# Kernel optimization log

Measured on AMD Instinct MI355X. Metric: run time of the kernel, lower is better.

## Reference

```python
import jax, jax.numpy as jnp
import numpy as np

EPS = 1e-06
K = 4          # hc_mult
D = 2048       # hidden_size
SINKHORN_ITERS = 20


def setup_inputs() -> dict:
    key = jax.random.key(0)
    k1, k2, k3 = jax.random.split(key, 3)
    B, S = 2, 4096
    x = jax.random.normal(k1, (B, S, K, D), dtype=jnp.float32)
    out = jax.random.normal(k2, (B, S, D), dtype=jnp.float32)
    out_dim = (2 + K) * K  # 24
    # matches nn.init.normal_(std=1/sqrt(K*D))
    W = jax.random.normal(k3, (out_dim, K * D), dtype=jnp.float32) / np.sqrt(K * D)
    scale = jnp.ones((3,), dtype=jnp.float32)
    base = jnp.zeros((out_dim,), dtype=jnp.float32)
    return {"x": x, "out": out, "W": W, "scale": scale, "base": base}


def _sinkhorn(m, n_iters=SINKHORN_ITERS, eps=EPS):
    # one priming column normalization, then (n_iters-1) row/col cycles
    m = m / (jnp.sum(m, axis=-2, keepdims=True) + eps)
    for _ in range(max(n_iters - 1, 0)):
        m = m / (jnp.sum(m, axis=-1, keepdims=True) + eps)
        m = m / (jnp.sum(m, axis=-2, keepdims=True) + eps)
    return m


def reference(x, out, W, scale, base):
    out_dtype = x.dtype
    # --- _packed_logits: flatten K streams, RMS-normalize, project (fp32) ---
    flat = x.reshape(*x.shape[:-2], K * D).astype(jnp.float32)      # [B,S,K*D]
    rsqrt = jax.lax.rsqrt(jnp.mean(flat * flat, axis=-1, keepdims=True) + EPS)
    logits = jnp.einsum('bsf,of->bso', flat * rsqrt, W)             # [B,S,24]
    # --- compute_weights: split into pre/post/comb ---
    pre_logit = logits[..., :K] * scale[0] + base[:K]
    post_logit = logits[..., K:2 * K] * scale[1] + base[K:2 * K]
    comb_logit = (logits[..., 2 * K:].reshape(*logits.shape[:-1], K, K) * scale[2]
                  + base[2 * K:].reshape(K, K))
    pre = jax.nn.sigmoid(pre_logit) + EPS                           # [B,S,K]
    post = 2.0 * jax.nn.sigmoid(post_logit)                         # [B,S,K]
    comb = jax.nn.softmax(comb_logit, axis=-1) + EPS                # [B,S,K,K]
    comb = _sinkhorn(comb)                                          # doubly-stochastic
    pre = pre.astype(out_dtype)
    post = post.astype(out_dtype)
    comb = comb.astype(out_dtype)
    # --- collapse: K streams -> 1 via pre weights ---
    collapsed = jnp.sum(pre[..., None] * x, axis=-2)                # [B,S,D]
    # --- expand: write sub-block output back to K streams ---
    write = post[..., None] * out[..., None, :]                     # [B,S,K,D]
    mix = jnp.einsum('bshk,bskd->bshd', comb, x)                    # [B,S,K,D]
    y = write + mix
    return (y, collapsed)
```

## Files before the change

### kernel.cpp

```cpp
#include <hip/hip_runtime.h>


#define EPS 1e-6f
constexpr int K_ = 4, D_ = 2048, KD = 8192, NOUT = 24;
constexpr int NTOK = 2 * 4096;
constexpr int TPB = 512;
constexpr int TOKS = 4;

typedef _Float16 h2 __attribute__((ext_vector_type(2)));

static __device__ __forceinline__ unsigned int pk2(float a, float b) {
    h2 h; h.x = (_Float16)a; h.y = (_Float16)b;
    return __builtin_bit_cast(unsigned int, h);
}

static __device__ __forceinline__ float dot2(unsigned int w, unsigned int x, float c) {
#if __has_builtin(__builtin_amdgcn_fdot2)
    return __builtin_amdgcn_fdot2(__builtin_bit_cast(h2, w),
                                  __builtin_bit_cast(h2, x), c, false);
#else
    h2 hw = __builtin_bit_cast(h2, w), hx = __builtin_bit_cast(h2, x);
    return c + (float)hw.x * (float)hx.x + (float)hw.y * (float)hx.y;
#endif
}

__global__ void conv_w_kernel(const float* __restrict__ W, unsigned int* __restrict__ Wh) {
    int g = blockIdx.x * blockDim.x + threadIdx.x;
    const float* src = W + (size_t)g * 8;
    float4 a = *reinterpret_cast<const float4*>(src);
    float4 b = *reinterpret_cast<const float4*>(src + 4);
    uint4 u;
    u.x = pk2(a.x, a.y); u.y = pk2(a.z, a.w);
    u.z = pk2(b.x, b.y); u.w = pk2(b.z, b.w);
    *reinterpret_cast<uint4*>(Wh + (size_t)g * 4) = u;
}

template <bool FH>
__global__ __launch_bounds__(TPB) void hypermix_kernel(
    const float* __restrict__ x, const float* __restrict__ outp,
    const unsigned int* __restrict__ Wh, const float* __restrict__ Wf,
    const float* __restrict__ scale, const float* __restrict__ base,
    float* __restrict__ y, float* __restrict__ coll)
{
    const int t = threadIdx.x;
    const int w = t >> 6, lane = t & 63;
    const int tk4 = t >> 7, t7 = t & 127;
    const size_t gt0 = (size_t)blockIdx.x * TOKS;

    __shared__ unsigned int xh[TOKS][KD / 2];
    __shared__ float ssred[8];
    __shared__ float lg[TOKS][24];
    __shared__ float wts[TOKS][24];

    {
        const float* xb = x + (gt0 + tk4) * KD + t7 * 4;
        float ss = 0.f;
#pragma unroll 2
        for (int i = 0; i < 16; ++i) {
            float4 v = *reinterpret_cast<const float4*>(xb + i * 512);
            ss += v.x * v.x + v.y * v.y + v.z * v.z + v.w * v.w;
            uint2 p; p.x = pk2(v.x, v.y); p.y = pk2(v.z, v.w);
            *reinterpret_cast<uint2*>(&xh[tk4][i * 256 + t7 * 2]) = p;
        }
#pragma unroll
        for (int m = 1; m < 64; m <<= 1) ss += __shfl_xor(ss, m, 64);
        if (lane == 0) ssred[w] = ss;
    }
    __syncthreads();

    {
        const int r0 = w * 3;
        float acc[3][4];
#pragma unroll
        for (int j = 0; j < 3; ++j)
#pragma unroll
            for (int tt = 0; tt < 4; ++tt) acc[j][tt] = 0.f;

#pragma unroll 2
        for (int it = 0; it < 16; ++it) {
            const int gi = it * 64 + lane;
            uint4 xv0 = *reinterpret_cast<const uint4*>(&xh[0][gi * 4]);
            uint4 xv1 = *reinterpret_cast<const uint4*>(&xh[1][gi * 4]);
            uint4 xv2 = *reinterpret_cast<const uint4*>(&xh[2][gi * 4]);
            uint4 xv3 = *reinterpret_cast<const uint4*>(&xh[3][gi * 4]);
#pragma unroll
            for (int j = 0; j < 3; ++j) {
                if (FH) {
                    uint4 wv = *reinterpret_cast<const uint4*>(
                        Wh + ((size_t)(r0 + j) * 4096 + gi * 4));
                    acc[j][0] = dot2(wv.x, xv0.x, acc[j][0]);
                    acc[j][0] = dot2(wv.y, xv0.y, acc[j][0]);
                    acc[j][0] = dot2(wv.z, xv0.z, acc[j][0]);
                    acc[j][0] = dot2(wv.w, xv0.w, acc[j][0]);
                    acc[j][1] = dot2(wv.x, xv1.x, acc[j][1]);
                    acc[j][1] = dot2(wv.y, xv1.y, acc[j][1]);
                    acc[j][1] = dot2(wv.z, xv1.z, acc[j][1]);
                    acc[j][1] = dot2(wv.w, xv1.w, acc[j][1]);
                    acc[j][2] = dot2(wv.x, xv2.x, acc[j][2]);
                    acc[j][2] = dot2(wv.y, xv2.y, acc[j][2]);
                    acc[j][2] = dot2(wv.z, xv2.z, acc[j][2]);
                    acc[j][2] = dot2(wv.w, xv2.w, acc[j][2]);
                    acc[j][3] = dot2(wv.x, xv3.x, acc[j][3]);
                    acc[j][3] = dot2(wv.y, xv3.y, acc[j][3]);
                    acc[j][3] = dot2(wv.z, xv3.z, acc[j][3]);
                    acc[j][3] = dot2(wv.w, xv3.w, acc[j][3]);
                } else {
                    const float* wr = Wf + (size_t)(r0 + j) * KD + gi * 8;
                    float4 w0 = *reinterpret_cast<const float4*>(wr);
                    float4 w1 = *reinterpret_cast<const float4*>(wr + 4);
                    unsigned int wa = pk2(w0.x, w0.y), wb = pk2(w0.z, w0.w);
                    unsigned int wc = pk2(w1.x, w1.y), wd = pk2(w1.z, w1.w);
                    acc[j][0] = dot2(wa, xv0.x, acc[j][0]);
                    acc[j][0] = dot2(wb, xv0.y, acc[j][0]);
                    acc[j][0] = dot2(wc, xv0.z, acc[j][0]);
                    acc[j][0] = dot2(wd, xv0.w, acc[j][0]);
                    acc[j][1] = dot2(wa, xv1.x, acc[j][1]);
                    acc[j][1] = dot2(wb, xv1.y, acc[j][1]);
                    acc[j][1] = dot2(wc, xv1.z, acc[j][1]);
                    acc[j][1] = dot2(wd, xv1.w, acc[j][1]);
                    acc[j][2] = dot2(wa, xv2.x, acc[j][2]);
                    acc[j][2] = dot2(wb, xv2.y, acc[j][2]);
                    acc[j][2] = dot2(wc, xv2.z, acc[j][2]);
                    acc[j][2] = dot2(wd, xv2.w, acc[j][2]);
                    acc[j][3] = dot2(wa, xv3.x, acc[j][3]);
                    acc[j][3] = dot2(wb, xv3.y, acc[j][3]);
                    acc[j][3] = dot2(wc, xv3.z, acc[j][3]);
                    acc[j][3] = dot2(wd, xv3.w, acc[j][3]);
                }
            }
        }
#pragma unroll
        for (int j = 0; j < 3; ++j)
#pragma unroll
            for (int tt = 0; tt < 4; ++tt) {
                float v = acc[j][tt];
#pragma unroll
                for (int m = 1; m < 64; m <<= 1) v += __shfl_xor(v, m, 64);
                if (lane == 0) lg[tt][r0 + j] = v;
            }
    }
    __syncthreads();

    if (t < 64) {
        const int wtk = t >> 4, idx = t & 15;
        float ss = ssred[2 * wtk] + ssred[2 * wtk + 1];
        float rms = rsqrtf(ss * (1.f / 8192.f) + EPS);
        float s0 = scale[0], s1 = scale[1], s2 = scale[2];
        float cl = lg[wtk][8 + idx] * rms * s2 + base[8 + idx];
        float mx = fmaxf(cl, __shfl_xor(cl, 1, 64));
        mx = fmaxf(mx, __shfl_xor(mx, 2, 64));
        float e = expf(cl - mx);
        float se = e + __shfl_xor(e, 1, 64); se += __shfl_xor(se, 2, 64);
        float m = e / se + EPS;
        float cs = m + __shfl_xor(m, 4, 64); cs += __shfl_xor(cs, 8, 64);
        m = m / (cs + EPS);
#pragma unroll 1
        for (int it = 0; it < 19; ++it) {
            float rs = m + __shfl_xor(m, 1, 64); rs += __shfl_xor(rs, 2, 64);
            m = m / (rs + EPS);
            cs = m + __shfl_xor(m, 4, 64); cs += __shfl_xor(cs, 8, 64);
            m = m / (cs + EPS);
        }
        wts[wtk][8 + idx] = m;
        if (idx < 4) {
            float z = lg[wtk][idx] * rms * s0 + base[idx];
            wts[wtk][idx] = 1.f / (1.f + expf(-z)) + EPS;
        } else if (idx < 8) {
            float z = lg[wtk][idx] * rms * s1 + base[idx];
            wts[wtk][idx] = 2.f / (1.f + expf(-z));
        }
    }
    __syncthreads();

    float pre[4], post[4], cmb[4][4];
#pragma unroll
    for (int k = 0; k < 4; ++k) { pre[k] = wts[tk4][k]; post[k] = wts[tk4][4 + k]; }
#pragma unroll
    for (int h = 0; h < 4; ++h)
#pragma unroll
        for (int k = 0; k < 4; ++k) cmb[h][k] = wts[tk4][8 + h * 4 + k];

    const float* ob = outp + (gt0 + tk4) * D_;
    float* yb = y + (gt0 + tk4) * KD;
    float* cb = coll + (gt0 + tk4) * D_;

#pragma unroll 1
    for (int dj = 0; dj < 4; ++dj) {
        const int d = dj * 512 + t7 * 4;
        float xk[4][4];
#pragma unroll
        for (int k = 0; k < 4; ++k) {
            uint2 p = *reinterpret_cast<const uint2*>(&xh[tk4][k * 1024 + (d >> 1)]);
            h2 h0 = __builtin_bit_cast(h2, p.x), h1 = __builtin_bit_cast(h2, p.y);
            xk[k][0] = (float)h0.x; xk[k][1] = (float)h0.y;
            xk[k][2] = (float)h1.x; xk[k][3] = (float)h1.y;
        }
        float4 ov = *reinterpret_cast<const float4*>(ob + d);
        float cv[4], yv[4];
#pragma unroll
        for (int e = 0; e < 4; ++e)
            cv[e] = pre[0] * xk[0][e] + pre[1] * xk[1][e]
                  + pre[2] * xk[2][e] + pre[3] * xk[3][e];
        *reinterpret_cast<float4*>(cb + d) = make_float4(cv[0], cv[1], cv[2], cv[3]);
        const float oe[4] = {ov.x, ov.y, ov.z, ov.w};
#pragma unroll
        for (int h = 0; h < 4; ++h) {
#pragma unroll
            for (int e = 0; e < 4; ++e)
                yv[e] = post[h] * oe[e] + cmb[h][0] * xk[0][e] + cmb[h][1] * xk[1][e]
                      + cmb[h][2] * xk[2][e] + cmb[h][3] * xk[3][e];
            *reinterpret_cast<float4*>(yb + h * D_ + d) =
                make_float4(yv[0], yv[1], yv[2], yv[3]);
        }
    }
}

extern "C" void kernel_launch(void* const* d_in, const int* in_sizes, int n_in,
                              void* d_out, int out_size, void* d_ws, size_t ws_size,
                              hipStream_t stream) {
    const float* x     = (const float*)d_in[0];
    const float* outp  = (const float*)d_in[1];
    const float* W     = (const float*)d_in[2];
    const float* scale = (const float*)d_in[3];
    const float* base  = (const float*)d_in[4];
    float* y    = (float*)d_out;
    float* coll = y + (size_t)NTOK * KD;

    const size_t wh_bytes = (size_t)NOUT * KD * 2;
    if (ws_size >= wh_bytes) {
        unsigned int* Wh = (unsigned int*)d_ws;
        conv_w_kernel<<<NOUT * KD / 8 / 256, 256, 0, stream>>>(W, Wh);
        hypermix_kernel<true><<<NTOK / TOKS, TPB, 0, stream>>>(x, outp, Wh, W, scale, base, y, coll);
    } else {
        hypermix_kernel<false><<<NTOK / TOKS, TPB, 0, stream>>>(x, outp, nullptr, W, scale, base, y, coll);
    }
}
```

Measured before the change: 181.0 us.

## Split fused hypermix kernel into logits, weights, and combine kernels

Breaks the single fused kernel into three: a logits kernel that writes projections and per-token sum-of-squares to a workspace, a per-thread weights kernel running softmax and Sinkhorn with fast reciprocal and exp, and a combine kernel that rereads x in fp32 from global memory. The combine step now uses full-precision x instead of the fp16 copy kept in shared memory, and the Sinkhorn loop no longer runs on only 64 threads while the rest of each block waits at a barrier. The cost is reading x twice from HBM (about 268 MB instead of 134 MB) plus extra launches. The workspace-size fallback is also removed.

```diff
diff --git a/kernel.cpp b/kernel.cpp
--- a/kernel.cpp
+++ b/kernel.cpp
@@ -2,10 +2,11 @@
 
 
 #define EPS 1e-6f
-constexpr int K_ = 4, D_ = 2048, KD = 8192, NOUT = 24;
-constexpr int NTOK = 2 * 4096;
+constexpr int D_ = 2048, KD = 8192, NOUT = 24;
+constexpr int NTOK = 8192;
 constexpr int TPB = 512;
 constexpr int TOKS = 4;
+constexpr int NBLK1 = NTOK / TOKS;
 
 typedef _Float16 h2 __attribute__((ext_vector_type(2)));
 
@@ -21,6 +22,14 @@
 #else
     h2 hw = __builtin_bit_cast(h2, w), hx = __builtin_bit_cast(h2, x);
     return c + (float)hw.x * (float)hx.x + (float)hw.y * (float)hx.y;
+#endif
+}
+
+static __device__ __forceinline__ float frcp(float v) {
+#if __has_builtin(__builtin_amdgcn_rcpf)
+    return __builtin_amdgcn_rcpf(v);
+#else
+    return 1.f / v;
 #endif
 }
 
@@ -35,12 +44,9 @@
     *reinterpret_cast<uint4*>(Wh + (size_t)g * 4) = u;
 }
 
-template <bool FH>
-__global__ __launch_bounds__(TPB) void hypermix_kernel(
-    const float* __restrict__ x, const float* __restrict__ outp,
-    const unsigned int* __restrict__ Wh, const float* __restrict__ Wf,
-    const float* __restrict__ scale, const float* __restrict__ base,
-    float* __restrict__ y, float* __restrict__ coll)
+__global__ __launch_bounds__(TPB) void logits_kernel(
+    const float* __restrict__ x, const unsigned int* __restrict__ Wh,
+    float* __restrict__ lgw)
 {
     const int t = threadIdx.x;
     const int w = t >> 6, lane = t & 63;
@@ -49,8 +55,6 @@
 
     __shared__ unsigned int xh[TOKS][KD / 2];
     __shared__ float ssred[8];
-    __shared__ float lg[TOKS][24];
-    __shared__ float wts[TOKS][24];
 
     {
         const float* xb = x + (gt0 + tk4) * KD + t7 * 4;
@@ -68,6 +72,9 @@
     }
     __syncthreads();
 
+    if (t < TOKS)
+        lgw[(gt0 + t) * 32 + 24] = ssred[2 * t] + ssred[2 * t + 1];
+
     {
         const int r0 = w * 3;
         float acc[3][4];
@@ -85,48 +92,24 @@
             uint4 xv3 = *reinterpret_cast<const uint4*>(&xh[3][gi * 4]);
 #pragma unroll
             for (int j = 0; j < 3; ++j) {
-                if (FH) {
-                    uint4 wv = *reinterpret_cast<const uint4*>(
-                        Wh + ((size_t)(r0 + j) * 4096 + gi * 4));
-                    acc[j][0] = dot2(wv.x, xv0.x, acc[j][0]);
-                    acc[j][0] = dot2(wv.y, xv0.y, acc[j][0]);
-                    acc[j][0] = dot2(wv.z, xv0.z, acc[j][0]);
-                    acc[j][0] = dot2(wv.w, xv0.w, acc[j][0]);
-                    acc[j][1] = dot2(wv.x, xv1.x, acc[j][1]);
-                    acc[j][1] = dot2(wv.y, xv1.y, acc[j][1]);
-                    acc[j][1] = dot2(wv.z, xv1.z, acc[j][1]);
-                    acc[j][1] = dot2(wv.w, xv1.w, acc[j][1]);
-                    acc[j][2] = dot2(wv.x, xv2.x, acc[j][2]);
-                    acc[j][2] = dot2(wv.y, xv2.y, acc[j][2]);
-                    acc[j][2] = dot2(wv.z, xv2.z, acc[j][2]);
-                    acc[j][2] = dot2(wv.w, xv2.w, acc[j][2]);
-                    acc[j][3] = dot2(wv.x, xv3.x, acc[j][3]);
-                    acc[j][3] = dot2(wv.y, xv3.y, acc[j][3]);
-                    acc[j][3] = dot2(wv.z, xv3.z, acc[j][3]);
-                    acc[j][3] = dot2(wv.w, xv3.w, acc[j][3]);
-                } else {
-                    const float* wr = Wf + (size_t)(r0 + j) * KD + gi * 8;
-                    float4 w0 = *reinterpret_cast<const float4*>(wr);
-                    float4 w1 = *reinterpret_cast<const float4*>(wr + 4);
-                    unsigned int wa = pk2(w0.x, w0.y), wb = pk2(w0.z, w0.w);
-                    unsigned int wc = pk2(w1.x, w1.y), wd = pk2(w1.z, w1.w);
-                    acc[j][0] = dot2(wa, xv0.x, acc[j][0]);
-                    acc[j][0] = dot2(wb, xv0.y, acc[j][0]);
-                    acc[j][0] = dot2(wc, xv0.z, acc[j][0]);
-                    acc[j][0] = dot2(wd, xv0.w, acc[j][0]);
-                    acc[j][1] = dot2(wa, xv1.x, acc[j][1]);
-                    acc[j][1] = dot2(wb, xv1.y, acc[j][1]);
-                    acc[j][1] = dot2(wc, xv1.z, acc[j][1]);
-                    acc[j][1] = dot2(wd, xv1.w, acc[j][1]);
-                    acc[j][2] = dot2(wa, xv2.x, acc[j][2]);
-                    acc[j][2] = dot2(wb, xv2.y, acc[j][2]);
-                    acc[j][2] = dot2(wc, xv2.z, acc[j][2]);
-                    acc[j][2] = dot2(wd, xv2.w, acc[j][2]);
-                    acc[j][3] = dot2(wa, xv3.x, acc[j][3]);
-                    acc[j][3] = dot2(wb, xv3.y, acc[j][3]);
-                    acc[j][3] = dot2(wc, xv3.z, acc[j][3]);
-                    acc[j][3] = dot2(wd, xv3.w, acc[j][3]);
-                }
+                uint4 wv = *reinterpret_cast<const uint4*>(
+                    Wh + ((size_t)(r0 + j) * 4096 + gi * 4));
+                acc[j][0] = dot2(wv.x, xv0.x, acc[j][0]);
+                acc[j][0] = dot2(wv.y, xv0.y, acc[j][0]);
+                acc[j][0] = dot2(wv.z, xv0.z, acc[j][0]);
+                acc[j][0] = dot2(wv.w, xv0.w, acc[j][0]);
+                acc[j][1] = dot2(wv.x, xv1.x, acc[j][1]);
+                acc[j][1] = dot2(wv.y, xv1.y, acc[j][1]);
+                acc[j][1] = dot2(wv.z, xv1.z, acc[j][1]);
+                acc[j][1] = dot2(wv.w, xv1.w, acc[j][1]);
+                acc[j][2] = dot2(wv.x, xv2.x, acc[j][2]);
+                acc[j][2] = dot2(wv.y, xv2.y, acc[j][2]);
+                acc[j][2] = dot2(wv.z, xv2.z, acc[j][2]);
+                acc[j][2] = dot2(wv.w, xv2.w, acc[j][2]);
+                acc[j][3] = dot2(wv.x, xv3.x, acc[j][3]);
+                acc[j][3] = dot2(wv.y, xv3.y, acc[j][3]);
+                acc[j][3] = dot2(wv.z, xv3.z, acc[j][3]);
+                acc[j][3] = dot2(wv.w, xv3.w, acc[j][3]);
             }
         }
 #pragma unroll
@@ -136,82 +119,121 @@
                 float v = acc[j][tt];
 #pragma unroll
                 for (int m = 1; m < 64; m <<= 1) v += __shfl_xor(v, m, 64);
-                if (lane == 0) lg[tt][r0 + j] = v;
+                if (lane == 0) lgw[(gt0 + tt) * 32 + r0 + j] = v;
             }
     }
+}
+
+__global__ __launch_bounds__(256) void weights_kernel(
+    float* __restrict__ lgw,
+    const float* __restrict__ scale, const float* __restrict__ base)
+{
+    const int tok = blockIdx.x * 256 + threadIdx.x;
+    if (tok >= NTOK) return;
+    float l[25];
+#pragma unroll
+    for (int i = 0; i < 25; ++i) l[i] = lgw[(size_t)tok * 32 + i];
+    float rms = rsqrtf(l[24] * (1.f / 8192.f) + EPS);
+    float s0 = scale[0], s1 = scale[1], s2 = scale[2];
+    float o[8];
+#pragma unroll
+    for (int k = 0; k < 4; ++k) {
+        float z0 = l[k] * rms * s0 + base[k];
+        o[k] = frcp(1.f + __expf(-z0)) + EPS;
+        float z1 = l[4 + k] * rms * s1 + base[4 + k];
+        o[4 + k] = 2.f * frcp(1.f + __expf(-z1));
+    }
+    float p[16];
+#pragma unroll
+    for (int h = 0; h < 4; ++h) {
+        float c0 = l[8 + h * 4 + 0] * rms * s2 + base[8 + h * 4 + 0];
+        float c1 = l[8 + h * 4 + 1] * rms * s2 + base[8 + h * 4 + 1];
+        float c2 = l[8 + h * 4 + 2] * rms * s2 + base[8 + h * 4 + 2];
+        float c3 = l[8 + h * 4 + 3] * rms * s2 + base[8 + h * 4 + 3];
+        float mx = fmaxf(fmaxf(c0, c1), fmaxf(c2, c3));
+        float e0 = __expf(c0 - mx), e1 = __expf(c1 - mx);
+        float e2 = __expf(c2 - mx), e3 = __expf(c3 - mx);
+        float inv = frcp(e0 + e1 + e2 + e3);
+        p[h * 4 + 0] = e0 * inv + EPS; p[h * 4 + 1] = e1 * inv + EPS;
+        p[h * 4 + 2] = e2 * inv + EPS; p[h * 4 + 3] = e3 * inv + EPS;
+    }
+#pragma unroll
+    for (int k = 0; k < 4; ++k) {
+        float inv = frcp(p[k] + p[4 + k] + p[8 + k] + p[12 + k] + EPS);
+        p[k] *= inv; p[4 + k] *= inv; p[8 + k] *= inv; p[12 + k] *= inv;
+    }
+#pragma unroll 1
+    for (int itn = 0; itn < 19; ++itn) {
+#pragma unroll
+        for (int h = 0; h < 4; ++h) {
+            float inv = frcp(p[h * 4] + p[h * 4 + 1] + p[h * 4 + 2] + p[h * 4 + 3] + EPS);
+            p[h * 4] *= inv; p[h * 4 + 1] *= inv; p[h * 4 + 2] *= inv; p[h * 4 + 3] *= inv;
+        }
+#pragma unroll
+        for (int k = 0; k < 4; ++k) {
+            float inv = frcp(p[k] + p[4 + k] + p[8 + k] + p[12 + k] + EPS);
+            p[k] *= inv; p[4 + k] *= inv; p[8 + k] *= inv; p[12 + k] *= inv;
+        }
+    }
+#pragma unroll
+    for (int i = 0; i < 8; ++i) lgw[(size_t)tok * 32 + i] = o[i];
+#pragma unroll
+    for (int i = 0; i < 16; ++i) lgw[(size_t)tok * 32 + 8 + i] = p[i];
+}
+
+__global__ __launch_bounds__(TPB) void combine_kernel(
+    const float* __restrict__ x, const float* __restrict__ outp,
+    const float* __restrict__ lgw,
+    float* __restrict__ y, float* __restrict__ coll)
+{
+    const int t = threadIdx.x;
+    const size_t tok = blockIdx.x;
+
+    __shared__ float wl[NOUT];
+    if (t < NOUT) wl[t] = lgw[tok * 32 + t];
     __syncthreads();
 
-    if (t < 64) {
-        const int wtk = t >> 4, idx = t & 15;
-        float ss = ssred[2 * wtk] + ssred[2 * wtk + 1];
-        float rms = rsqrtf(ss * (1.f / 8192.f) + EPS);
-        float s0 = scale[0], s1 = scale[1], s2 = scale[2];
-        float cl = lg[wtk][8 + idx] * rms * s2 + base[8 + idx];
-        float mx = fmaxf(cl, __shfl_xor(cl, 1, 64));
-        mx = fmaxf(mx, __shfl_xor(mx, 2, 64));
-        float e = expf(cl - mx);
-        float se = e + __shfl_xor(e, 1, 64); se += __shfl_xor(se, 2, 64);
-        float m = e / se + EPS;
-        float cs = m + __shfl_xor(m, 4, 64); cs += __shfl_xor(cs, 8, 64);
-        m = m / (cs + EPS);
-#pragma unroll 1
-        for (int it = 0; it < 19; ++it) {
-            float rs = m + __shfl_xor(m, 1, 64); rs += __shfl_xor(rs, 2, 64);
-            m = m / (rs + EPS);
-            cs = m + __shfl_xor(m, 4, 64); cs += __shfl_xor(cs, 8, 64);
-            m = m / (cs + EPS);
-        }
-        wts[wtk][8 + idx] = m;
-        if (idx < 4) {
-            float z = lg[wtk][idx] * rms * s0 + base[idx];
-            wts[wtk][idx] = 1.f / (1.f + expf(-z)) + EPS;
-        } else if (idx < 8) {
-            float z = lg[wtk][idx] * rms * s1 + base[idx];
-            wts[wtk][idx] = 2.f / (1.f + expf(-z));
-        }
-    }
-    __syncthreads();
+    const int d = t * 4;
+    const float* xb = x + tok * KD + d;
+    float4 xk[4];
+#pragma unroll
+    for (int k = 0; k < 4; ++k)
+        xk[k] = *reinterpret_cast<const float4*>(xb + k * D_);
+    float4 ov = *reinterpret_cast<const float4*>(outp + tok * D_ + d);
 
     float pre[4], post[4], cmb[4][4];
 #pragma unroll
-    for (int k = 0; k < 4; ++k) { pre[k] = wts[tk4][k]; post[k] = wts[tk4][4 + k]; }
+    for (int k = 0; k < 4; ++k) { pre[k] = wl[k]; post[k] = wl[4 + k]; }
 #pragma unroll
     for (int h = 0; h < 4; ++h)
 #pragma unroll
-        for (int k = 0; k < 4; ++k) cmb[h][k] = wts[tk4][8 + h * 4 + k];
-
-    const float* ob = outp + (gt0 + tk4) * D_;
-    float* yb = y + (gt0 + tk4) * KD;
-    float* cb = coll + (gt0 + tk4) * D_;
-
-#pragma unroll 1
-    for (int dj = 0; dj < 4; ++dj) {
-        const int d = dj * 512 + t7 * 4;
-        float xk[4][4];
-#pragma unroll
-        for (int k = 0; k < 4; ++k) {
-            uint2 p = *reinterpret_cast<const uint2*>(&xh[tk4][k * 1024 + (d >> 1)]);
-            h2 h0 = __builtin_bit_cast(h2, p.x), h1 = __builtin_bit_cast(h2, p.y);
-            xk[k][0] = (float)h0.x; xk[k][1] = (float)h0.y;
-            xk[k][2] = (float)h1.x; xk[k][3] = (float)h1.y;
-        }
-        float4 ov = *reinterpret_cast<const float4*>(ob + d);
-        float cv[4], yv[4];
+        for (int k = 0; k < 4; ++k) cmb[h][k] = wl[8 + h * 4 + k];
+
+    const float xe[4][4] = {
+        {xk[0].x, xk[0].y, xk[0].z, xk[0].w},
+        {xk[1].x, xk[1].y, xk[1].z, xk[1].w},
+        {xk[2].x, xk[2].y, xk[2].z, xk[2].w},
+        {xk[3].x, xk[3].y, xk[3].z, xk[3].w}};
+    const float oe[4] = {ov.x, ov.y, ov.z, ov.w};
+
+    float cv[4];
+#pragma unroll
+    for (int e = 0; e < 4; ++e)
+        cv[e] = pre[0] * xe[0][e] + pre[1] * xe[1][e]
+              + pre[2] * xe[2][e] + pre[3] * xe[3][e];
+    *reinterpret_cast<float4*>(coll + tok * D_ + d) =
+        make_float4(cv[0], cv[1], cv[2], cv[3]);
+
+    float* yb = y + tok * KD + d;
+#pragma unroll
+    for (int h = 0; h < 4; ++h) {
+        float yv[4];
 #pragma unroll
         for (int e = 0; e < 4; ++e)
-            cv[e] = pre[0] * xk[0][e] + pre[1] * xk[1][e]
-                  + pre[2] * xk[2][e] + pre[3] * xk[3][e];
-        *reinterpret_cast<float4*>(cb + d) = make_float4(cv[0], cv[1], cv[2], cv[3]);
-        const float oe[4] = {ov.x, ov.y, ov.z, ov.w};
-#pragma unroll
-        for (int h = 0; h < 4; ++h) {
-#pragma unroll
-            for (int e = 0; e < 4; ++e)
-                yv[e] = post[h] * oe[e] + cmb[h][0] * xk[0][e] + cmb[h][1] * xk[1][e]
-                      + cmb[h][2] * xk[2][e] + cmb[h][3] * xk[3][e];
-            *reinterpret_cast<float4*>(yb + h * D_ + d) =
-                make_float4(yv[0], yv[1], yv[2], yv[3]);
-        }
+            yv[e] = post[h] * oe[e] + cmb[h][0] * xe[0][e] + cmb[h][1] * xe[1][e]
+                  + cmb[h][2] * xe[2][e] + cmb[h][3] * xe[3][e];
+        *reinterpret_cast<float4*>(yb + h * D_) =
+            make_float4(yv[0], yv[1], yv[2], yv[3]);
     }
 }
 
@@ -226,12 +248,11 @@
     float* y    = (float*)d_out;
     float* coll = y + (size_t)NTOK * KD;
 
-    const size_t wh_bytes = (size_t)NOUT * KD * 2;
-    if (ws_size >= wh_bytes) {
-        unsigned int* Wh = (unsigned int*)d_ws;
-        conv_w_kernel<<<NOUT * KD / 8 / 256, 256, 0, stream>>>(W, Wh);
-        hypermix_kernel<true><<<NTOK / TOKS, TPB, 0, stream>>>(x, outp, Wh, W, scale, base, y, coll);
-    } else {
-        hypermix_kernel<false><<<NTOK / TOKS, TPB, 0, stream>>>(x, outp, nullptr, W, scale, base, y, coll);
-    }
-}
+    unsigned int* Wh = (unsigned int*)d_ws;
+    float* lgw = (float*)((char*)d_ws + (size_t)NOUT * KD * 2);
+
+    conv_w_kernel<<<NOUT * KD / 8 / 256, 256, 0, stream>>>(W, Wh);
+    logits_kernel<<<NBLK1, TPB, 0, stream>>>(x, Wh, lgw);
+    weights_kernel<<<NTOK / 256, 256, 0, stream>>>(lgw, scale, base);
+    combine_kernel<<<NTOK, TPB, 0, stream>>>(x, outp, lgw, y, coll);
+}
```

Measured after the change: 217.9 us. 1.2x slower.
